# Optimization experiments

Hardware: AMD Instinct MI355X
Metric: run time of the kernel (lower is better)

The kernel has to match this reference:

```python
import jax, jax.numpy as jnp
from jax import lax
import numpy as np

B, T, F, H, MH = 512, 256, 8, 128, 512  # batch, horizon, exo features, lstm hidden, mlp hidden


def setup_inputs() -> dict:
    key = jax.random.key(0)
    ks = jax.random.split(key, 32)

    def u(k, shape, scale):
        return jax.random.uniform(k, shape, jnp.float32, -scale, scale)

    kH = 1.0 / np.sqrt(H)
    kM = 1.0 / np.sqrt(MH)
    inp = {}
    for i, n in enumerate(["Dis_out", "Dis_rad", "Dis_occ"]):
        inp[n] = jax.random.normal(ks[i], (B, T, F), jnp.float32)
    for j in range(3):
        b = 3 + j * 5
        inp[f"lstm{j+1}_Wih"] = u(ks[b], (4 * H, F), kH)      # torch gate order i,f,g,o
        inp[f"lstm{j+1}_Whh"] = u(ks[b + 1], (4 * H, H), kH)
        inp[f"lstm{j+1}_b"] = u(ks[b + 2], (4 * H,), kH)
        inp[f"lstm{j+1}_hw"] = u(ks[b + 3], (H,), kH)          # linear head H -> 1
        inp[f"lstm{j+1}_hb"] = u(ks[b + 4], (), kH)
    inp["mlp_W1"] = u(ks[20], (3, MH), 1.0 / np.sqrt(3.0))
    inp["mlp_b1"] = u(ks[21], (MH,), 1.0 / np.sqrt(3.0))
    inp["mlp_W2"] = u(ks[22], (MH, MH), kM)
    inp["mlp_b2"] = u(ks[23], (MH,), kM)
    inp["mlp_W3"] = u(ks[24], (MH,), kM)
    inp["mlp_b3"] = u(ks[25], (), kM)
    return inp


def _lstm_head(x, Wih, Whh, b, hw, hb):
    # x: (B,T,F) -> per-step scalar prediction (B,T)
    Bsz, Hs = x.shape[0], Whh.shape[1]

    def step(carry, xt):
        h, c = carry
        z = xt @ Wih.T + h @ Whh.T + b                 # (B,4H)
        i, f, g, o = jnp.split(z, 4, axis=-1)
        c = jax.nn.sigmoid(f) * c + jax.nn.sigmoid(i) * jnp.tanh(g)
        h = jax.nn.sigmoid(o) * jnp.tanh(c)
        return (h, c), h

    h0 = jnp.zeros((Bsz, Hs), x.dtype)
    _, hs = lax.scan(step, (h0, h0), jnp.swapaxes(x, 0, 1))  # hs: (T,B,H)
    return jnp.einsum('tbh,h->bt', hs, hw) + hb              # (B,T)


def reference(Dis_out, Dis_rad, Dis_occ,
              lstm1_Wih, lstm1_Whh, lstm1_b, lstm1_hw, lstm1_hb,
              lstm2_Wih, lstm2_Whh, lstm2_b, lstm2_hw, lstm2_hb,
              lstm3_Wih, lstm3_Whh, lstm3_b, lstm3_hw, lstm3_hb,
              mlp_W1, mlp_b1, mlp_W2, mlp_b2, mlp_W3, mlp_b3):
    D1 = _lstm_head(Dis_out, lstm1_Wih, lstm1_Whh, lstm1_b, lstm1_hw, lstm1_hb)
    D2 = _lstm_head(Dis_rad, lstm2_Wih, lstm2_Whh, lstm2_b, lstm2_hw, lstm2_hb)
    D3 = _lstm_head(Dis_occ, lstm3_Wih, lstm3_Whh, lstm3_b, lstm3_hw, lstm3_hb)
    # Batched replacement of the per-timestep loop: concat -> tiny MLP, all T at once.
    x = jnp.stack([D1, D2, D3], axis=-1)                      # (B,T,3)
    h = jax.nn.relu(x @ mlp_W1 + mlp_b1)                      # (B,T,MH)
    h = jax.nn.relu(h @ mlp_W2 + mlp_b2)                      # (B,T,MH)
    c_p_F = h @ mlp_W3 + mlp_b3                               # (B,T)
    return (D1, D2, D3, c_p_F)
```

## Files before the change

### kernel.cpp

```cpp
#include <hip/hip_runtime.h>

#define B_ 512
#define T_ 256
#define F_ 8
#define H_ 128
#define BT_ (B_*T_)
#define MH_ 512
#define L2E 1.4426950408889634f

typedef __attribute__((ext_vector_type(4))) float f32x4;
typedef __attribute__((ext_vector_type(8))) __bf16 bf16x8;

__device__ unsigned short g_w2t[MH_*MH_];
__device__ unsigned short g_whh[3][512][128];
__device__ unsigned short g_wih[3][512][32];
__device__ unsigned short g_xbf[3][B_*T_*F_];

__device__ __forceinline__ unsigned short f2bf(float f){
  unsigned int u = __float_as_uint(f);
  unsigned int r = (u + 0x7FFFu + ((u >> 16) & 1u)) >> 16;
  return (unsigned short)r;
}

#if __has_builtin(__builtin_amdgcn_exp2f)
#define EXP2F __builtin_amdgcn_exp2f
#else
#define EXP2F exp2f
#endif
#define RCPF __builtin_amdgcn_rcpf

template<int CTRL>
__device__ __forceinline__ float dpp_sum_step(float v){
  int t = __builtin_amdgcn_update_dpp(0, __float_as_int(v), CTRL, 0xF, 0xF, true);
  return v + __int_as_float(t);
}

struct LstmArgs {
  const float* x[3];
  const float* Wih[3];
  const float* Whh[3];
  const float* bias[3];
  const float* hw[3];
  const float* hb[3];
  float* out;
};

__global__ __launch_bounds__(256) void prep_all(LstmArgs A, const float* __restrict__ W2){
  const int NW2 = MH_*MH_;
  const int NW  = 3*512*128;
  const int NI  = 3*512*32;
  const int NX  = 3*B_*T_*F_;
  const int TOT = NW2 + NW + NI + NX;
  for (int i = blockIdx.x*256 + threadIdx.x; i < TOT; i += gridDim.x*256){
    if (i < NW2){
      int n = i >> 9;
      int k = i & 511;
      g_w2t[(n << 9) | (k ^ ((n & 7) << 3))] = f2bf(W2[(size_t)k * MH_ + n]);
    } else if (i < NW2 + NW){
      int j = i - NW2;
      int head = j >> 16;
      int r = j & 65535;
      int pc = r >> 7, k = r & 127;
      int w = pc >> 6, g = (pc >> 4) & 3, s = pc & 15;
      int row = g*128 + w*16 + s;
      float sc = (g == 2) ? (2.0f*L2E) : (-L2E);
      g_whh[head][pc][k] = f2bf(A.Whh[head][row*H_ + k] * sc);
    } else if (i < NW2 + NW + NI){
      int j = i - NW2 - NW;
      int head = j >> 14;
      int r = j & 16383;
      int pc = r >> 5, k = r & 31;
      int w = pc >> 6, g = (pc >> 4) & 3, s = pc & 15;
      int row = g*128 + w*16 + s;
      float sc = (g == 2) ? (2.0f*L2E) : (-L2E);
      g_wih[head][pc][k] = (k < 8) ? f2bf(A.Wih[head][row*F_ + k] * sc) : (unsigned short)0;
    } else {
      int j = i - NW2 - NW - NI;
      int head = j >> 20;
      int r = j & 1048575;
      g_xbf[head][r] = f2bf(A.x[head][r]);
    }
  }
}

__global__ __launch_bounds__(512) void lstm_mfma_kernel(LstmArgs A){
  const int head   = blockIdx.x >> 6;
  const int batch0 = (blockIdx.x & 63) * 8;
  const int tid = threadIdx.x;
  const int w   = tid >> 6;
  const int l   = tid & 63;
  const int c16 = l & 15;
  const int kb  = (l >> 4) * 8;

  const float* __restrict__ bs  = A.bias[head];
  const float* __restrict__ hwp = A.hw[head];
  const float hbv = A.hb[head][0];
  float* __restrict__ D = A.out + (size_t)head * BT_;

  bf16x8 bh[4][4];
  bf16x8 bx[4];
  #pragma unroll
  for (int g = 0; g < 4; ++g){
    const int pc = w*64 + g*16 + c16;
    #pragma unroll
    for (int kk = 0; kk < 4; ++kk)
      bh[g][kk] = *(const bf16x8*)&g_whh[head][pc][kk*32 + kb];
    bx[g] = *(const bf16x8*)&g_wih[head][pc][kb];
  }

  const int u = w*16 + c16;
  const float bi_ = bs[u]        * (-L2E);
  const float bf_ = bs[H_+u]     * (-L2E);
  const float bg_ = bs[2*H_+u]   * (2.0f*L2E);
  const float bo_ = bs[3*H_+u]   * (-L2E);
  const float hw_u = hwp[u];

  __shared__ __align__(16) unsigned short h_bf[2][16][132];
  __shared__ float part[2][8][8];

  for (int i = tid; i < 2*16*132; i += 512) ((unsigned short*)h_bf)[i] = 0;

  float cst[2] = {0.f, 0.f};
  float pp[2]  = {0.f, 0.f};

  const int bt = ((c16 >> 2) << 1) | (c16 & 1);
  const bool xvalid = (l < 16) && !(l & 2);
  const unsigned short* __restrict__ xrow =
      &g_xbf[head][(size_t)(batch0 + bt) * (T_*F_)];

  bf16x8 ax_cur = {};
  if (xvalid) ax_cur = *(const bf16x8*)(xrow);

  __syncthreads();

  int cur = 0;
  for (int ts = 0; ts < T_; ++ts){
    bf16x8 ah[4];
    #pragma unroll
    for (int kk = 0; kk < 4; ++kk)
      ah[kk] = *(const bf16x8*)&h_bf[cur][c16][kk*32 + kb];

    bf16x8 ax_nxt = {};
    {
      const int tn = (ts + 1 < T_) ? ts + 1 : ts;
      if (xvalid) ax_nxt = *(const bf16x8*)(xrow + tn*F_);
    }

    f32x4 acc[4];
    const f32x4 z4 = {0.f, 0.f, 0.f, 0.f};
    #pragma unroll
    for (int g = 0; g < 4; ++g)
      acc[g] = __builtin_amdgcn_mfma_f32_16x16x32_bf16(ah[0], bh[g][0], z4, 0, 0, 0);
    #pragma unroll
    for (int kk = 1; kk < 4; ++kk){
      #pragma unroll
      for (int g = 0; g < 4; ++g)
        acc[g] = __builtin_amdgcn_mfma_f32_16x16x32_bf16(ah[kk], bh[g][kk], acc[g], 0, 0, 0);
    }
    #pragma unroll
    for (int g = 0; g < 4; ++g)
      acc[g] = __builtin_amdgcn_mfma_f32_16x16x32_bf16(ax_cur, bx[g], acc[g], 0, 0, 0);

    if (ts > 0){
      #pragma unroll
      for (int r = 0; r < 2; ++r){
        float v = pp[r];
        v = dpp_sum_step<0xB1>(v);
        v = dpp_sum_step<0x4E>(v);
        v = dpp_sum_step<0x141>(v);
        v = dpp_sum_step<0x140>(v);
        if (c16 == 0) part[(ts-1) & 1][(l >> 4)*2 + r][w] = v;
      }
    }

    #pragma unroll
    for (int r = 0; r < 2; ++r){
      const float Zi = acc[0][r] + bi_;
      const float Zf = acc[1][r] + bf_;
      const float Zg = acc[2][r] + bg_;
      const float Zo = acc[3][r] + bo_;
      const float si = RCPF(1.f + EXP2F(Zi));
      const float sf = RCPF(1.f + EXP2F(Zf));
      const float tg = 1.f - 2.f * RCPF(EXP2F(Zg) + 1.f);
      const float so = RCPF(1.f + EXP2F(Zo));
      cst[r] = sf * cst[r] + si * tg;
      const float tc = 1.f - 2.f * RCPF(EXP2F(cst[r] * (2.0f*L2E)) + 1.f);
      const float hnr = so * tc;
      h_bf[cur ^ 1][(l >> 4)*4 + r][u] = f2bf(hnr);
      pp[r] = hnr * hw_u;
    }

    __syncthreads();

    if (ts > 0 && tid < 64){
      const int b  = tid >> 3;
      const int wv = tid & 7;
      float v = part[(ts-1) & 1][b][wv];
      v = dpp_sum_step<0xB1>(v);
      v = dpp_sum_step<0x4E>(v);
      v = dpp_sum_step<0x141>(v);
      if (wv == 0) D[(size_t)(batch0 + b) * T_ + (ts-1)] = v + hbv;
    }

    ax_cur = ax_nxt;
    cur ^= 1;
  }

  #pragma unroll
  for (int r = 0; r < 2; ++r){
    float v = pp[r];
    v = dpp_sum_step<0xB1>(v);
    v = dpp_sum_step<0x4E>(v);
    v = dpp_sum_step<0x141>(v);
    v = dpp_sum_step<0x140>(v);
    if (c16 == 0) part[(T_-1) & 1][(l >> 4)*2 + r][w] = v;
  }
  __syncthreads();
  if (tid < 64){
    const int b  = tid >> 3;
    const int wv = tid & 7;
    float v = part[(T_-1) & 1][b][wv];
    v = dpp_sum_step<0xB1>(v);
    v = dpp_sum_step<0x4E>(v);
    v = dpp_sum_step<0x141>(v);
    if (wv == 0) D[(size_t)(batch0 + b) * T_ + (T_-1)] = v + hbv;
  }
}

__global__ __launch_bounds__(256, 2) void mlp_kernel(
    const float* __restrict__ Dbase,
    const float* __restrict__ W1, const float* __restrict__ b1,
    const float* __restrict__ b2, const float* __restrict__ W3,
    const float* __restrict__ b3, float* __restrict__ out)
{
  __shared__ __align__(16) unsigned short buf[2][32*512];

  const int tid = threadIdx.x;
  const int l   = tid & 63;
  const int c16 = l & 15;
  const int kb  = (l >> 4) * 8;
  const int w   = tid >> 6;
  const int m0  = blockIdx.x * 128 + w * 32;

  bf16x8 afr[2][16];
  {
    float d[2][3];
    #pragma unroll
    for (int mt = 0; mt < 2; ++mt){
      const int gr = m0 + mt*16 + c16;
      d[mt][0] = Dbase[gr];
      d[mt][1] = Dbase[BT_ + gr];
      d[mt][2] = Dbase[2*BT_ + gr];
    }
    #pragma unroll
    for (int ks = 0; ks < 16; ++ks){
      const int kg = ks*32 + kb;
      const f32x4 wa0 = *(const f32x4*)(W1 + kg);          const f32x4 wa1 = *(const f32x4*)(W1 + kg + 4);
      const f32x4 wb0 = *(const f32x4*)(W1 + MH_ + kg);    const f32x4 wb1 = *(const f32x4*)(W1 + MH_ + kg + 4);
      const f32x4 wc0 = *(const f32x4*)(W1 + 2*MH_ + kg);  const f32x4 wc1 = *(const f32x4*)(W1 + 2*MH_ + kg + 4);
      const f32x4 bv0 = *(const f32x4*)(b1 + kg);          const f32x4 bv1 = *(const f32x4*)(b1 + kg + 4);
      #pragma unroll
      for (int mt = 0; mt < 2; ++mt){
        union { unsigned short us[8]; bf16x8 v; } au;
        #pragma unroll
        for (int i = 0; i < 4; ++i){
          float v0 = fmaf(d[mt][2], wc0[i], fmaf(d[mt][1], wb0[i], fmaf(d[mt][0], wa0[i], bv0[i])));
          float v1 = fmaf(d[mt][2], wc1[i], fmaf(d[mt][1], wb1[i], fmaf(d[mt][0], wa1[i], bv1[i])));
          au.us[i]     = f2bf(fmaxf(v0, 0.f));
          au.us[4 + i] = f2bf(fmaxf(v1, 0.f));
        }
        afr[mt][ks] = au.v;
      }
    }
  }

  const uint4* __restrict__ gsrc = (const uint4*)g_w2t;
  uint4 rg0, rg1, rg2, rg3, rg4, rg5, rg6, rg7;
  {
    const uint4* s = gsrc + tid;
    rg0 = s[0*256]; rg1 = s[1*256]; rg2 = s[2*256]; rg3 = s[3*256];
    rg4 = s[4*256]; rg5 = s[5*256]; rg6 = s[6*256]; rg7 = s[7*256];
  }

  float rs[2][4] = {{0.f,0.f,0.f,0.f},{0.f,0.f,0.f,0.f}};

  #pragma unroll 1
  for (int p = 0; p < 16; ++p){
    {
      uint4* bw = (uint4*)buf[p & 1] + tid;
      bw[0*256] = rg0; bw[1*256] = rg1; bw[2*256] = rg2; bw[3*256] = rg3;
      bw[4*256] = rg4; bw[5*256] = rg5; bw[6*256] = rg6; bw[7*256] = rg7;
    }
    __syncthreads();
    if (p < 15){
      const uint4* s = gsrc + (p + 1) * 2048 + tid;
      rg0 = s[0*256]; rg1 = s[1*256]; rg2 = s[2*256]; rg3 = s[3*256];
      rg4 = s[4*256]; rg5 = s[5*256]; rg6 = s[6*256]; rg7 = s[7*256];
    }
    float b2v[2], w3v[2];
    #pragma unroll
    for (int nt = 0; nt < 2; ++nt){
      const int n = p*32 + nt*16 + c16;
      b2v[nt] = b2[n];
      w3v[nt] = W3[n];
    }

    const unsigned short* __restrict__ bb = buf[p & 1];
    f32x4 acc[2][2];
    #pragma unroll
    for (int nt = 0; nt < 2; ++nt){
      f32x4 z = {0.f,0.f,0.f,0.f};
      acc[0][nt] = z; acc[1][nt] = z;
    }
    #pragma unroll
    for (int ks = 0; ks < 16; ++ks){
      #pragma unroll
      for (int nt = 0; nt < 2; ++nt){
        const int nl = nt*16 + c16;
        const bf16x8 bfr =
          *(const bf16x8*)&bb[(nl << 9) | ((ks*32 + kb) ^ ((nl & 7) << 3))];
        acc[0][nt] = __builtin_amdgcn_mfma_f32_16x16x32_bf16(afr[0][ks], bfr, acc[0][nt], 0, 0, 0);
        acc[1][nt] = __builtin_amdgcn_mfma_f32_16x16x32_bf16(afr[1][ks], bfr, acc[1][nt], 0, 0, 0);
      }
    }
    #pragma unroll
    for (int nt = 0; nt < 2; ++nt){
      #pragma unroll
      for (int mt = 0; mt < 2; ++mt)
        #pragma unroll
        for (int r = 0; r < 4; ++r)
          rs[mt][r] += fmaxf(acc[mt][nt][r] + b2v[nt], 0.f) * w3v[nt];
    }
  }

  #pragma unroll
  for (int mt = 0; mt < 2; ++mt){
    #pragma unroll
    for (int r = 0; r < 4; ++r){
      rs[mt][r] += __shfl_xor(rs[mt][r], 1);
      rs[mt][r] += __shfl_xor(rs[mt][r], 2);
      rs[mt][r] += __shfl_xor(rs[mt][r], 4);
      rs[mt][r] += __shfl_xor(rs[mt][r], 8);
    }
  }
  if (c16 == 0){
    const float bv = b3[0];
    #pragma unroll
    for (int mt = 0; mt < 2; ++mt){
      const int row = m0 + mt*16 + (l >> 4) * 4;
      #pragma unroll
      for (int r = 0; r < 4; ++r)
        out[3*BT_ + row + r] = rs[mt][r] + bv;
    }
  }
}

extern "C" void kernel_launch(void* const* d_in, const int* in_sizes, int n_in,
                              void* d_out, int out_size, void* d_ws, size_t ws_size,
                              hipStream_t stream){
  LstmArgs A;
  for (int i = 0; i < 3; ++i){
    A.x[i]    = (const float*)d_in[i];
    A.Wih[i]  = (const float*)d_in[3 + i*5 + 0];
    A.Whh[i]  = (const float*)d_in[3 + i*5 + 1];
    A.bias[i] = (const float*)d_in[3 + i*5 + 2];
    A.hw[i]   = (const float*)d_in[3 + i*5 + 3];
    A.hb[i]   = (const float*)d_in[3 + i*5 + 4];
  }
  A.out = (float*)d_out;

  prep_all<<<dim3(2048), dim3(256), 0, stream>>>(A, (const float*)d_in[20]);
  lstm_mfma_kernel<<<dim3(192), dim3(512), 0, stream>>>(A);
  mlp_kernel<<<dim3(1024), dim3(256), 0, stream>>>((const float*)d_out,
      (const float*)d_in[18], (const float*)d_in[19],
      (const float*)d_in[21], (const float*)d_in[22], (const float*)d_in[23],
      (float*)d_out);
}
```

Measured before the change: 281.6 us.

## Batch LSTM head reductions over 8 steps and rotate finalizing wave

Widens the partial-sum buffer to a 16-step ring so the cross-wave reduction of the linear head no longer runs every timestep behind a single wave. Every 8 steps one wave, chosen in rotation, reads 8 steps of partials with vector LDS loads and writes 8 outputs. The per-step __syncthreads is replaced by an explicit lgkmcnt wait plus s_barrier. This is meant to take the serialized tail work of wave 0 off the recurrent critical path, at the cost of a larger LDS buffer and delicate ring-index correctness.

```diff
diff --git a/kernel.cpp b/kernel.cpp
--- a/kernel.cpp
+++ b/kernel.cpp
@@ -33,6 +33,10 @@
 __device__ __forceinline__ float dpp_sum_step(float v){
   int t = __builtin_amdgcn_update_dpp(0, __float_as_int(v), CTRL, 0xF, 0xF, true);
   return v + __int_as_float(t);
+}
+
+__device__ __forceinline__ void bar_lgkm(){
+  asm volatile("s_waitcnt lgkmcnt(0)\n\ts_barrier" ::: "memory");
 }
 
 struct LstmArgs {
@@ -116,7 +120,7 @@
   const float hw_u = hwp[u];
 
   __shared__ __align__(16) unsigned short h_bf[2][16][132];
-  __shared__ float part[2][8][8];
+  __shared__ __align__(16) float part[16][8][8];
 
   for (int i = tid; i < 2*16*132; i += 512) ((unsigned short*)h_bf)[i] = 0;
 
@@ -169,8 +173,18 @@
         v = dpp_sum_step<0x4E>(v);
         v = dpp_sum_step<0x141>(v);
         v = dpp_sum_step<0x140>(v);
-        if (c16 == 0) part[(ts-1) & 1][(l >> 4)*2 + r][w] = v;
+        if (c16 == 0) part[(ts-1) & 15][(l >> 4)*2 + r][w] = v;
       }
+    }
+
+    if ((ts & 7) == 1 && ts >= 9 && w == ((ts >> 3) & 7)){
+      const int s = (ts - 9) + (l >> 3);
+      const int b = l & 7;
+      const f32x4 pa = *(const f32x4*)&part[s & 15][b][0];
+      const f32x4 pb = *(const f32x4*)&part[s & 15][b][4];
+      const float v = ((pa[0]+pa[1]) + (pa[2]+pa[3]))
+                    + ((pb[0]+pb[1]) + (pb[2]+pb[3]));
+      D[(size_t)(batch0 + b) * T_ + s] = v + hbv;
     }
 
     #pragma unroll
@@ -190,17 +204,7 @@
       pp[r] = hnr * hw_u;
     }
 
-    __syncthreads();
-
-    if (ts > 0 && tid < 64){
-      const int b  = tid >> 3;
-      const int wv = tid & 7;
-      float v = part[(ts-1) & 1][b][wv];
-      v = dpp_sum_step<0xB1>(v);
-      v = dpp_sum_step<0x4E>(v);
-      v = dpp_sum_step<0x141>(v);
-      if (wv == 0) D[(size_t)(batch0 + b) * T_ + (ts-1)] = v + hbv;
-    }
+    bar_lgkm();
 
     ax_cur = ax_nxt;
     cur ^= 1;
@@ -213,17 +217,17 @@
     v = dpp_sum_step<0x4E>(v);
     v = dpp_sum_step<0x141>(v);
     v = dpp_sum_step<0x140>(v);
-    if (c16 == 0) part[(T_-1) & 1][(l >> 4)*2 + r][w] = v;
+    if (c16 == 0) part[(T_-1) & 15][(l >> 4)*2 + r][w] = v;
   }
   __syncthreads();
-  if (tid < 64){
-    const int b  = tid >> 3;
-    const int wv = tid & 7;
-    float v = part[(T_-1) & 1][b][wv];
-    v = dpp_sum_step<0xB1>(v);
-    v = dpp_sum_step<0x4E>(v);
-    v = dpp_sum_step<0x141>(v);
-    if (wv == 0) D[(size_t)(batch0 + b) * T_ + (T_-1)] = v + hbv;
+  if (w == 0){
+    const int s = (T_ - 8) + (l >> 3);
+    const int b = l & 7;
+    const f32x4 pa = *(const f32x4*)&part[s & 15][b][0];
+    const f32x4 pb = *(const f32x4*)&part[s & 15][b][4];
+    const float v = ((pa[0]+pa[1]) + (pa[2]+pa[3]))
+                  + ((pb[0]+pb[1]) + (pb[2]+pb[3]));
+    D[(size_t)(batch0 + b) * T_ + s] = v + hbv;
   }
 }
 
```

Result: slower. 292.2 us (+3.8%).

## Halve batch rows per LSTM block to double grid and shorten per-step work

Applied to the files above, without the earlier changes.

Each LSTM workgroup now handles 4 batch rows instead of 8, so the grid grows from 192 to 384 blocks and spreads the serial recurrence over more CUs. Each lane now computes one gate row per step instead of two, which shortens the sequential per-step chain, though MFMA tiles are only a quarter used (one row per 4-row group). The head reduction is rotated across waves by timestep so no single wave always pays for it. The cost is more wasted MFMA throughput and weight loads repeated across twice as many blocks.

```diff
diff --git a/kernel.cpp b/kernel.cpp
--- a/kernel.cpp
+++ b/kernel.cpp
@@ -84,8 +84,8 @@
 }
 
 __global__ __launch_bounds__(512) void lstm_mfma_kernel(LstmArgs A){
-  const int head   = blockIdx.x >> 6;
-  const int batch0 = (blockIdx.x & 63) * 8;
+  const int head   = blockIdx.x >> 7;
+  const int batch0 = (blockIdx.x & 127) * 4;
   const int tid = threadIdx.x;
   const int w   = tid >> 6;
   const int l   = tid & 63;
@@ -116,15 +116,15 @@
   const float hw_u = hwp[u];
 
   __shared__ __align__(16) unsigned short h_bf[2][16][132];
-  __shared__ float part[2][8][8];
+  __shared__ float part[2][4][8];
 
   for (int i = tid; i < 2*16*132; i += 512) ((unsigned short*)h_bf)[i] = 0;
 
-  float cst[2] = {0.f, 0.f};
-  float pp[2]  = {0.f, 0.f};
-
-  const int bt = ((c16 >> 2) << 1) | (c16 & 1);
-  const bool xvalid = (l < 16) && !(l & 2);
+  float cst = 0.f;
+  float pp  = 0.f;
+
+  const int bt = c16 >> 2;
+  const bool xvalid = (l < 16) && ((l & 3) == 0);
   const unsigned short* __restrict__ xrow =
       &g_xbf[head][(size_t)(batch0 + bt) * (T_*F_)];
 
@@ -162,39 +162,35 @@
       acc[g] = __builtin_amdgcn_mfma_f32_16x16x32_bf16(ax_cur, bx[g], acc[g], 0, 0, 0);
 
     if (ts > 0){
-      #pragma unroll
-      for (int r = 0; r < 2; ++r){
-        float v = pp[r];
-        v = dpp_sum_step<0xB1>(v);
-        v = dpp_sum_step<0x4E>(v);
-        v = dpp_sum_step<0x141>(v);
-        v = dpp_sum_step<0x140>(v);
-        if (c16 == 0) part[(ts-1) & 1][(l >> 4)*2 + r][w] = v;
-      }
-    }
-
-    #pragma unroll
-    for (int r = 0; r < 2; ++r){
-      const float Zi = acc[0][r] + bi_;
-      const float Zf = acc[1][r] + bf_;
-      const float Zg = acc[2][r] + bg_;
-      const float Zo = acc[3][r] + bo_;
+      float v = pp;
+      v = dpp_sum_step<0xB1>(v);
+      v = dpp_sum_step<0x4E>(v);
+      v = dpp_sum_step<0x141>(v);
+      v = dpp_sum_step<0x140>(v);
+      if (c16 == 0) part[(ts-1) & 1][l >> 4][w] = v;
+    }
+
+    {
+      const float Zi = acc[0][0] + bi_;
+      const float Zf = acc[1][0] + bf_;
+      const float Zg = acc[2][0] + bg_;
+      const float Zo = acc[3][0] + bo_;
       const float si = RCPF(1.f + EXP2F(Zi));
       const float sf = RCPF(1.f + EXP2F(Zf));
       const float tg = 1.f - 2.f * RCPF(EXP2F(Zg) + 1.f);
       const float so = RCPF(1.f + EXP2F(Zo));
-      cst[r] = sf * cst[r] + si * tg;
-      const float tc = 1.f - 2.f * RCPF(EXP2F(cst[r] * (2.0f*L2E)) + 1.f);
+      cst = sf * cst + si * tg;
+      const float tc = 1.f - 2.f * RCPF(EXP2F(cst * (2.0f*L2E)) + 1.f);
       const float hnr = so * tc;
-      h_bf[cur ^ 1][(l >> 4)*4 + r][u] = f2bf(hnr);
-      pp[r] = hnr * hw_u;
+      h_bf[cur ^ 1][(l >> 4)*4][u] = f2bf(hnr);
+      pp = hnr * hw_u;
     }
 
     __syncthreads();
 
-    if (ts > 0 && tid < 64){
-      const int b  = tid >> 3;
-      const int wv = tid & 7;
+    if (ts > 0 && w == (ts & 7) && l < 32){
+      const int b  = l >> 3;
+      const int wv = l & 7;
       float v = part[(ts-1) & 1][b][wv];
       v = dpp_sum_step<0xB1>(v);
       v = dpp_sum_step<0x4E>(v);
@@ -206,17 +202,16 @@
     cur ^= 1;
   }
 
-  #pragma unroll
-  for (int r = 0; r < 2; ++r){
-    float v = pp[r];
+  {
+    float v = pp;
     v = dpp_sum_step<0xB1>(v);
     v = dpp_sum_step<0x4E>(v);
     v = dpp_sum_step<0x141>(v);
     v = dpp_sum_step<0x140>(v);
-    if (c16 == 0) part[(T_-1) & 1][(l >> 4)*2 + r][w] = v;
+    if (c16 == 0) part[(T_-1) & 1][l >> 4][w] = v;
   }
   __syncthreads();
-  if (tid < 64){
+  if (tid < 32){
     const int b  = tid >> 3;
     const int wv = tid & 7;
     float v = part[(T_-1) & 1][b][wv];
@@ -370,7 +365,7 @@
   A.out = (float*)d_out;
 
   prep_all<<<dim3(2048), dim3(256), 0, stream>>>(A, (const float*)d_in[20]);
-  lstm_mfma_kernel<<<dim3(192), dim3(512), 0, stream>>>(A);
+  lstm_mfma_kernel<<<dim3(384), dim3(512), 0, stream>>>(A);
   mlp_kernel<<<dim3(1024), dim3(256), 0, stream>>>((const float*)d_out,
       (const float*)d_in[18], (const float*)d_in[19],
       (const float*)d_in[21], (const float*)d_in[22], (const float*)d_in[23],
```

Result: slower. 388.9 us (+38.1%).
